# Optimization experiments

Hardware: AMD Instinct MI355X
Metric: run time of the kernel (lower is better)

Reference implementation:

```python
import jax, jax.numpy as jnp
import numpy as np

N_NODES = 50000
N_EDGES = 1600000
H1, F1 = 6, 16   # conv1 heads/filters
H2, F2 = 6, 24   # conv2 heads/filters
D_IN = 11
NEG_SLOPE = 0.2
EPS = 1e-12


def gat_layer(x, src, dst, W, a_src, a_dst, heads, filt):
    # x: [N, Din], W: [Din, heads*filt], a_src/a_dst: [heads, filt]
    N = x.shape[0]
    h = (x @ W).reshape(N, heads, filt)                      # [N,H,F]
    alpha_s = jnp.einsum('nhf,hf->nh', h, a_src)             # [N,H]
    alpha_d = jnp.einsum('nhf,hf->nh', h, a_dst)             # [N,H]
    e = jax.nn.leaky_relu(alpha_s[src] + alpha_d[dst], NEG_SLOPE)  # [E,H]
    # softmax over incoming edges of each dst node (segment softmax)
    m = jax.ops.segment_max(e, dst, num_segments=N)          # [N,H]
    m = jnp.where(jnp.isfinite(m), m, 0.0)
    ex = jnp.exp(e - m[dst])                                 # [E,H]
    denom = jax.ops.segment_sum(ex, dst, num_segments=N)     # [N,H]
    att = ex / (denom[dst] + EPS)                            # [E,H]
    msg = h[src] * att[:, :, None]                           # [E,H,F]
    out = jax.ops.segment_sum(msg, dst, num_segments=N)      # [N,H,F]
    return jax.nn.elu(out).reshape(N, heads * filt)


def setup_inputs() -> dict:
    key = jax.random.key(0)
    ks = jax.random.split(key, 12)
    x = jax.random.normal(ks[0], (N_NODES, D_IN), dtype=jnp.float32)
    src = jax.random.randint(ks[1], (N_EDGES,), 0, N_NODES, dtype=jnp.int32)
    dst = jax.random.randint(ks[2], (N_EDGES,), 0, N_NODES, dtype=jnp.int32)
    s = 0.1
    W1 = jax.random.normal(ks[3], (D_IN, H1 * F1), dtype=jnp.float32) * s
    a1s = jax.random.normal(ks[4], (H1, F1), dtype=jnp.float32) * s
    a1d = jax.random.normal(ks[5], (H1, F1), dtype=jnp.float32) * s
    W2 = jax.random.normal(ks[6], (H1 * F1, H2 * F2), dtype=jnp.float32) * s
    a2s = jax.random.normal(ks[7], (H2, F2), dtype=jnp.float32) * s
    a2d = jax.random.normal(ks[8], (H2, F2), dtype=jnp.float32) * s
    Wd = jax.random.normal(ks[9], (H2 * F2, 1), dtype=jnp.float32) * s
    bd = jnp.zeros((1,), dtype=jnp.float32)
    return {"x": x, "src": src, "dst": dst, "W1": W1, "a1s": a1s, "a1d": a1d,
            "W2": W2, "a2s": a2s, "a2d": a2d, "Wd": Wd, "bd": bd}


def reference(x, src, dst, W1, a1s, a1d, W2, a2s, a2d, Wd, bd):
    h = gat_layer(x, src, dst, W1, a1s, a1d, H1, F1)   # [N, 96]
    h = gat_layer(h, src, dst, W2, a2s, a2d, H2, F2)   # [N, 144]
    pooled = jnp.sum(h, axis=0).reshape(1, -1)         # [1, 144]
    norm = jnp.sqrt(jnp.sum(pooled * pooled, axis=1, keepdims=True))
    pooled = pooled / jnp.maximum(norm, 1e-12)         # F.normalize
    out = pooled @ Wd + bd                             # [1, 1], linear nonlin
    return jnp.squeeze(out, axis=1)                    # [1]
```

## Files before the change

kernel.cpp:

```cpp
#include <hip/hip_runtime.h>
#include <math.h>

#define NNODES 50000
#define NEDGES 1600000
#define NB 391
#define NBP 400

__device__ __forceinline__ float lrelu(float v) { return v > 0.f ? v : 0.2f * v; }

template<int SEL>
__device__ __forceinline__ float fp8d(unsigned u) {
    return __builtin_amdgcn_cvt_f32_fp8((int)u, SEL);
}

__global__ void prep_kernel(const float* __restrict__ x, float* __restrict__ xp,
                            const float* __restrict__ W1, const float* __restrict__ a1s,
                            const float* __restrict__ a1d, float* __restrict__ va1s,
                            float* __restrict__ va1d,
                            const float* __restrict__ W2, const float* __restrict__ a2s,
                            const float* __restrict__ a2d, float* __restrict__ va2s,
                            float* __restrict__ va2d,
                            int* __restrict__ bcnt, float* __restrict__ pooled, int N) {
    int b = blockIdx.x, t = threadIdx.x;
    if (b == 0) {
        if (t < 96) {
            int k = t >> 3, h = t & 7;
            float s = 0.f, d = 0.f;
            if (h < 6 && k < 11) {
                for (int f = 0; f < 16; ++f) {
                    float w = W1[k * 96 + h * 16 + f];
                    s = fmaf(w, a1s[h * 16 + f], s);
                    d = fmaf(w, a1d[h * 16 + f], d);
                }
            }
            va1s[t] = s;
            va1d[t] = d;
        }
    } else if (b == 1) {
        if (t < 768) {
            int k = t >> 3, h = t & 7;
            float s = 0.f, d = 0.f;
            if (h < 6) {
                for (int f = 0; f < 24; ++f) {
                    float w = W2[k * 144 + h * 24 + f];
                    s = fmaf(w, a2s[h * 24 + f], s);
                    d = fmaf(w, a2d[h * 24 + f], d);
                }
            }
            va2s[t] = s;
            va2d[t] = d;
        }
    } else if (b == 2) {
        if (t < NB) bcnt[t] = 0;
        if (t >= 512 && t < 512 + 144) pooled[t - 512] = 0.f;
    } else {
        int i = (b - 3) * 768 + t;
        if (i < N * 12) {
            int n = i / 12, k = i - n * 12;
            xp[i] = (k < 11) ? x[n * 11 + k] : 0.f;
        }
    }
}

template<int DIN>
__global__ void alphap_kernel(const float* __restrict__ X, const float* __restrict__ va_s,
                              const float* __restrict__ va_d, float* __restrict__ asp,
                              float* __restrict__ adp, int N) {
    __shared__ float vs[DIN * 8], vd[DIN * 8];
    for (int i = threadIdx.x; i < DIN * 8; i += blockDim.x) { vs[i] = va_s[i]; vd[i] = va_d[i]; }
    __syncthreads();
    int t = blockIdx.x * blockDim.x + threadIdx.x;
    if (t >= N * 8) return;
    int n = t / 8, h = t - n * 8;
    const float* xr = X + (size_t)n * DIN;
    float s = 0.f, d = 0.f;
    for (int k = 0; k < DIN; ++k) {
        float xv = xr[k];
        s = fmaf(xv, vs[k * 8 + h], s);
        d = fmaf(xv, vd[k * 8 + h], d);
    }
    asp[t] = s;
    adp[t] = d;
}

__global__ void bucket_hist_kernel(const int* __restrict__ dst, int* __restrict__ bcnt, int E) {
    __shared__ int h[NBP];
    for (int i = threadIdx.x; i < NBP; i += blockDim.x) h[i] = 0;
    __syncthreads();
    for (int e = blockIdx.x * blockDim.x + threadIdx.x; e < E; e += gridDim.x * blockDim.x)
        atomicAdd(&h[dst[e] >> 7], 1);
    __syncthreads();
    for (int i = threadIdx.x; i < NB; i += blockDim.x)
        if (h[i]) atomicAdd(&bcnt[i], h[i]);
}

__global__ void bucket_scan_kernel(const int* __restrict__ bcnt, int* __restrict__ bbase,
                                   int* __restrict__ bcur, int* __restrict__ off, int E) {
    __shared__ int ls[512];
    int t = threadIdx.x;
    int c = (t < NB) ? bcnt[t] : 0;
    ls[t] = c;
    __syncthreads();
    for (int o = 1; o < 512; o <<= 1) {
        int u = (t >= o) ? ls[t - o] : 0;
        __syncthreads();
        ls[t] += u;
        __syncthreads();
    }
    if (t < NB) {
        int ex = ls[t] - c;
        bbase[t] = ex;
        bcur[t] = ex;
    }
    if (t == 0) { bbase[NB] = E; off[NNODES] = E; }
}

#define BA_CHUNK 8192
#define BA_THREADS 1024
__global__ void binA_kernel(const int* __restrict__ src, const int* __restrict__ dst,
                            int* __restrict__ bcur, unsigned* __restrict__ tmp, int E) {
    __shared__ unsigned sv[BA_CHUNK];
    __shared__ unsigned short sb[BA_CHUNK];
    __shared__ int cnt[NBP], basel[NBP];
    int tid = threadIdx.x;
    for (int i = tid; i < NBP; i += BA_THREADS) cnt[i] = 0;
    __syncthreads();
    int e0 = blockIdx.x * BA_CHUNK;
    int lim = min(BA_CHUNK, E - e0);
#pragma unroll
    for (int k = 0; k < BA_CHUNK / BA_THREADS; ++k) {
        int i = k * BA_THREADS + tid;
        if (i < lim) {
            int s = src[e0 + i], d = dst[e0 + i];
            sv[i] = (unsigned)s | ((unsigned)(d & 127) << 17);
            int b = d >> 7;
            sb[i] = (unsigned short)b;
            atomicAdd(&cnt[b], 1);
        }
    }
    __syncthreads();
    for (int i = tid; i < NB; i += BA_THREADS)
        basel[i] = cnt[i] ? atomicAdd(&bcur[i], cnt[i]) : 0;
    __syncthreads();
#pragma unroll
    for (int k = 0; k < BA_CHUNK / BA_THREADS; ++k) {
        int i = k * BA_THREADS + tid;
        if (i < lim) {
            int pos = atomicAdd(&basel[sb[i]], 1);
            tmp[pos] = sv[i];
        }
    }
}

__global__ void binB_kernel(const int* __restrict__ bbase, const unsigned* __restrict__ tmp,
                            int* __restrict__ off, int* __restrict__ esrc, int N) {
    __shared__ int ncnt[128], ncur[128], ls[128];
    int b = blockIdx.x;
    int tid = threadIdx.x;
    int lo = bbase[b], hi = bbase[b + 1];
    if (tid < 128) ncnt[tid] = 0;
    __syncthreads();
    for (int i = lo + tid; i < hi; i += 256)
        atomicAdd(&ncnt[tmp[i] >> 17], 1);
    __syncthreads();
    if (tid < 128) ls[tid] = ncnt[tid];
    __syncthreads();
    for (int o = 1; o < 128; o <<= 1) {
        int u = (tid >= o && tid < 128) ? ls[tid - o] : 0;
        __syncthreads();
        if (tid < 128) ls[tid] += u;
        __syncthreads();
    }
    if (tid < 128) {
        int ex = lo + ls[tid] - ncnt[tid];
        int n = b * 128 + tid;
        if (n < N) off[n] = ex;
        ncur[tid] = ex;
    }
    __syncthreads();
    for (int i = lo + tid; i < hi; i += 256) {
        unsigned v = tmp[i];
        int pos = atomicAdd(&ncur[v >> 17], 1);
        esrc[pos] = (int)(v & 0x1FFFFu);
    }
}

#define G1_NODES 128
#define G1_THREADS (G1_NODES * 3)
#define G1_ECAP 4800
__global__ void gather1_kernel(const int* __restrict__ off, const int* __restrict__ esrc,
                               const float* __restrict__ asp, const float* __restrict__ adp,
                               const float* __restrict__ xp, float* __restrict__ aggX, int N) {
    __shared__ int se[G1_ECAP];
    int li = threadIdx.x;
    int n0 = blockIdx.x * G1_NODES;
    int nend = min(n0 + G1_NODES, N);
    int base = off[n0];
    int cnt = off[nend] - base;
    bool staged = (cnt <= G1_ECAP);
    if (staged) for (int i = li; i < cnt; i += G1_THREADS) se[i] = esrc[base + i];
    __syncthreads();
    int node = n0 + li / 3;
    int j = li % 3;
    if (node >= N) return;
    const float4 advA = *(const float4*)(adp + (size_t)node * 8);
    const float2 advB = *(const float2*)(adp + (size_t)node * 8 + 4);
    const float4* xp4 = (const float4*)xp;
    int p0 = off[node], p1 = off[node + 1];
    float4 ac[6];
    float d[6];
#pragma unroll
    for (int u = 0; u < 6; ++u) { ac[u] = make_float4(0.f, 0.f, 0.f, 0.f); d[u] = 0.f; }
#define G1_EDGE(asA, asB, xv)                                                        \
    {                                                                                \
        float a0 = __expf(lrelu(asA.x + advA.x));                                    \
        float a1 = __expf(lrelu(asA.y + advA.y));                                    \
        float a2 = __expf(lrelu(asA.z + advA.z));                                    \
        float a3 = __expf(lrelu(asA.w + advA.w));                                    \
        float a4 = __expf(lrelu(asB.x + advB.x));                                    \
        float a5 = __expf(lrelu(asB.y + advB.y));                                    \
        d[0] += a0; d[1] += a1; d[2] += a2; d[3] += a3; d[4] += a4; d[5] += a5;      \
        ac[0].x = fmaf(a0, xv.x, ac[0].x); ac[0].y = fmaf(a0, xv.y, ac[0].y);        \
        ac[0].z = fmaf(a0, xv.z, ac[0].z); ac[0].w = fmaf(a0, xv.w, ac[0].w);        \
        ac[1].x = fmaf(a1, xv.x, ac[1].x); ac[1].y = fmaf(a1, xv.y, ac[1].y);        \
        ac[1].z = fmaf(a1, xv.z, ac[1].z); ac[1].w = fmaf(a1, xv.w, ac[1].w);        \
        ac[2].x = fmaf(a2, xv.x, ac[2].x); ac[2].y = fmaf(a2, xv.y, ac[2].y);        \
        ac[2].z = fmaf(a2, xv.z, ac[2].z); ac[2].w = fmaf(a2, xv.w, ac[2].w);        \
        ac[3].x = fmaf(a3, xv.x, ac[3].x); ac[3].y = fmaf(a3, xv.y, ac[3].y);        \
        ac[3].z = fmaf(a3, xv.z, ac[3].z); ac[3].w = fmaf(a3, xv.w, ac[3].w);        \
        ac[4].x = fmaf(a4, xv.x, ac[4].x); ac[4].y = fmaf(a4, xv.y, ac[4].y);        \
        ac[4].z = fmaf(a4, xv.z, ac[4].z); ac[4].w = fmaf(a4, xv.w, ac[4].w);        \
        ac[5].x = fmaf(a5, xv.x, ac[5].x); ac[5].y = fmaf(a5, xv.y, ac[5].y);        \
        ac[5].z = fmaf(a5, xv.z, ac[5].z); ac[5].w = fmaf(a5, xv.w, ac[5].w);        \
    }
#define G1_LOOP(FS)                                                                  \
    {                                                                                \
        for (; q + 4 <= qe; q += 4) {                                                \
            int s0 = FS(q), s1 = FS(q + 1), s2 = FS(q + 2), s3 = FS(q + 3);          \
            float4 A0 = *(const float4*)(asp + (size_t)s0 * 8);                      \
            float2 B0 = *(const float2*)(asp + (size_t)s0 * 8 + 4);                  \
            float4 X0 = xp4[(size_t)s0 * 3 + j];                                     \
            float4 A1 = *(const float4*)(asp + (size_t)s1 * 8);                      \
            float2 B1 = *(const float2*)(asp + (size_t)s1 * 8 + 4);                  \
            float4 X1 = xp4[(size_t)s1 * 3 + j];                                     \
            float4 A2 = *(const float4*)(asp + (size_t)s2 * 8);                      \
            float2 B2 = *(const float2*)(asp + (size_t)s2 * 8 + 4);                  \
            float4 X2 = xp4[(size_t)s2 * 3 + j];                                     \
            float4 A3 = *(const float4*)(asp + (size_t)s3 * 8);                      \
            float2 B3 = *(const float2*)(asp + (size_t)s3 * 8 + 4);                  \
            float4 X3 = xp4[(size_t)s3 * 3 + j];                                     \
            G1_EDGE(A0, B0, X0) G1_EDGE(A1, B1, X1)                                  \
            G1_EDGE(A2, B2, X2) G1_EDGE(A3, B3, X3)                                  \
        }                                                                            \
        for (; q < qe; ++q) {                                                        \
            int s0 = FS(q);                                                          \
            float4 A0 = *(const float4*)(asp + (size_t)s0 * 8);                      \
            float2 B0 = *(const float2*)(asp + (size_t)s0 * 8 + 4);                  \
            float4 X0 = xp4[(size_t)s0 * 3 + j];                                     \
            G1_EDGE(A0, B0, X0)                                                      \
        }                                                                            \
    }
#define G1_SE(i) se[i]
#define G1_GE(i) esrc[i]
    if (staged) {
        int q = p0 - base, qe = p1 - base;
        G1_LOOP(G1_SE)
    } else {
        int q = p0, qe = p1;
        G1_LOOP(G1_GE)
    }
#undef G1_EDGE
#undef G1_LOOP
    float4* o4 = (float4*)aggX;
#pragma unroll
    for (int u = 0; u < 6; ++u) {
        float r = 1.f / (d[u] + 1e-12f);
        float4 a = ac[u];
        a.x *= r; a.y *= r; a.z *= r; a.w *= r;
        o4[((size_t)node * 6 + u) * 3 + j] = a;
    }
}

__global__ void gemmL1_kernel(const float* __restrict__ aggX, const float* __restrict__ W1,
                              float* __restrict__ out1, int N) {
    __shared__ float Wl[12 * 96];
    for (int i = threadIdx.x; i < 12 * 96; i += blockDim.x) Wl[i] = (i < 11 * 96) ? W1[i] : 0.f;
    __syncthreads();
    int t = blockIdx.x * blockDim.x + threadIdx.x;
    if (t >= N * 24) return;
    int n = t / 24, q = t - n * 24;
    int h = q / 4, c = q * 4;
    const float* ag = aggX + ((size_t)n * 6 + h) * 12;
    float4 acc = {0, 0, 0, 0};
#pragma unroll
    for (int k = 0; k < 12; ++k) {
        float xv = ag[k];
        acc.x = fmaf(xv, Wl[k * 96 + c + 0], acc.x);
        acc.y = fmaf(xv, Wl[k * 96 + c + 1], acc.y);
        acc.z = fmaf(xv, Wl[k * 96 + c + 2], acc.z);
        acc.w = fmaf(xv, Wl[k * 96 + c + 3], acc.w);
    }
    acc.x = acc.x > 0.f ? acc.x : expm1f(acc.x);
    acc.y = acc.y > 0.f ? acc.y : expm1f(acc.y);
    acc.z = acc.z > 0.f ? acc.z : expm1f(acc.z);
    acc.w = acc.w > 0.f ? acc.w : expm1f(acc.w);
    ((float4*)out1)[(size_t)n * 24 + q] = acc;
}

template<int DIN, int C, int NPT>
__global__ void gemm_fp8_kernel(const float* __restrict__ X, const float* __restrict__ W,
                                unsigned* __restrict__ Out, int N) {
    constexpr int Q = C / 4;
    __shared__ float4 Wl[DIN * Q];
    for (int i = threadIdx.x; i < DIN * Q; i += blockDim.x) Wl[i] = ((const float4*)W)[i];
    __syncthreads();
    int t = blockIdx.x * blockDim.x + threadIdx.x;
    int g = t / Q, q = t - g * Q;
    int n0 = g * NPT;
    if (n0 >= N) return;
    const float4* X4 = (const float4*)X;
    float4 acc[NPT];
#pragma unroll
    for (int u = 0; u < NPT; ++u) acc[u] = make_float4(0.f, 0.f, 0.f, 0.f);
#pragma unroll 2
    for (int k4 = 0; k4 < DIN / 4; ++k4) {
        float4 xv[NPT];
#pragma unroll
        for (int u = 0; u < NPT; ++u) xv[u] = X4[(size_t)(n0 + u) * (DIN / 4) + k4];
#pragma unroll
        for (int i = 0; i < 4; ++i) {
            float4 w = Wl[(k4 * 4 + i) * Q + q];
#pragma unroll
            for (int u = 0; u < NPT; ++u) {
                float xs = (i == 0) ? xv[u].x : (i == 1) ? xv[u].y : (i == 2) ? xv[u].z : xv[u].w;
                acc[u].x = fmaf(xs, w.x, acc[u].x);
                acc[u].y = fmaf(xs, w.y, acc[u].y);
                acc[u].z = fmaf(xs, w.z, acc[u].z);
                acc[u].w = fmaf(xs, w.w, acc[u].w);
            }
        }
    }
#pragma unroll
    for (int u = 0; u < NPT; ++u) {
        int pk = __builtin_amdgcn_cvt_pk_fp8_f32(acc[u].x, acc[u].y, 0, false);
        pk     = __builtin_amdgcn_cvt_pk_fp8_f32(acc[u].z, acc[u].w, pk, true);
        Out[(size_t)(n0 + u) * Q + q] = (unsigned)pk;
    }
}

#define G2_NODES 28
#define G2_TPN 18
#define G2_THREADS 512
#define G2_ACTIVE (G2_NODES * G2_TPN)
#define G2_ECAP 1600
__global__ void gather2_kernel(const int* __restrict__ off, const int* __restrict__ esrc,
                               const float* __restrict__ asp, const float* __restrict__ adp,
                               const uint2* __restrict__ h2t2, float* __restrict__ pooled, int N) {
    __shared__ float sp[144];
    __shared__ int se[G2_ECAP];
    int li = threadIdx.x;
    int n0 = blockIdx.x * G2_NODES;
    int nend = min(n0 + G2_NODES, N);
    int base = off[n0];
    int cnt = off[nend] - base;
    bool staged = (cnt <= G2_ECAP);
    if (staged) for (int i = li; i < cnt; i += G2_THREADS) se[i] = esrc[base + i];
    if (li < 144) sp[li] = 0.f;
    __syncthreads();
    int node = n0 + li / G2_TPN;
    int j = li % G2_TPN;
    if (li < G2_ACTIVE && node < N) {
        int h = j / 3;
        float adv = adp[(size_t)node * 8 + h];
        int p0 = off[node], p1 = off[node + 1];
        float acc[8];
#pragma unroll
        for (int c = 0; c < 8; ++c) acc[c] = 0.f;
        float den = 0.f;
#define G2_EDGE(ev, v)                                                     \
    {                                                                      \
        float att = __expf(lrelu(ev + adv));                               \
        den += att;                                                        \
        acc[0] = fmaf(att, fp8d<0>(v.x), acc[0]);                          \
        acc[1] = fmaf(att, fp8d<1>(v.x), acc[1]);                          \
        acc[2] = fmaf(att, fp8d<2>(v.x), acc[2]);                          \
        acc[3] = fmaf(att, fp8d<3>(v.x), acc[3]);                          \
        acc[4] = fmaf(att, fp8d<0>(v.y), acc[4]);                          \
        acc[5] = fmaf(att, fp8d<1>(v.y), acc[5]);                          \
        acc[6] = fmaf(att, fp8d<2>(v.y), acc[6]);                          \
        acc[7] = fmaf(att, fp8d<3>(v.y), acc[7]);                          \
    }
#define G2_LOOP(FS)                                                                        \
    {                                                                                      \
        for (; q + 4 <= qe; q += 4) {                                                      \
            int s0 = FS(q), s1 = FS(q + 1), s2 = FS(q + 2), s3 = FS(q + 3);                \
            float e0 = asp[(size_t)s0 * 8 + h], e1 = asp[(size_t)s1 * 8 + h];              \
            float e2 = asp[(size_t)s2 * 8 + h], e3 = asp[(size_t)s3 * 8 + h];              \
            uint2 v0 = h2t2[(size_t)s0 * 18 + j], v1 = h2t2[(size_t)s1 * 18 + j];          \
            uint2 v2 = h2t2[(size_t)s2 * 18 + j], v3 = h2t2[(size_t)s3 * 18 + j];          \
            G2_EDGE(e0, v0) G2_EDGE(e1, v1) G2_EDGE(e2, v2) G2_EDGE(e3, v3)                \
        }                                                                                  \
        for (; q < qe; ++q) {                                                              \
            int s0 = FS(q);                                                                \
            float e0 = asp[(size_t)s0 * 8 + h];                                            \
            uint2 v0 = h2t2[(size_t)s0 * 18 + j];                                          \
            G2_EDGE(e0, v0)                                                                \
        }                                                                                  \
    }
#define G2_SE(i) se[i]
#define G2_GE(i) esrc[i]
        if (staged) {
            int q = p0 - base, qe = p1 - base;
            G2_LOOP(G2_SE)
        } else {
            int q = p0, qe = p1;
            G2_LOOP(G2_GE)
        }
#undef G2_EDGE
#undef G2_LOOP
        float rd = 1.f / (den + 1e-12f);
        int cb = 8 * j;
#pragma unroll
        for (int c = 0; c < 8; ++c) {
            float vv = acc[c] * rd;
            vv = vv > 0.f ? vv : expm1f(vv);
            atomicAdd(&sp[cb + c], vv);
        }
    }
    __syncthreads();
    if (li < 144) atomicAdd(&pooled[li], sp[li]);
}

__global__ void final_kernel(const float* __restrict__ pooled, const float* __restrict__ Wd,
                             const float* __restrict__ bd, float* __restrict__ out) {
    int l = threadIdx.x;
    float ss = 0.f, dot = 0.f;
    for (int c = l; c < 144; c += 64) {
        float p = pooled[c];
        ss = fmaf(p, p, ss);
        dot = fmaf(p, Wd[c], dot);
    }
#pragma unroll
    for (int o = 32; o > 0; o >>= 1) {
        ss += __shfl_down(ss, o);
        dot += __shfl_down(dot, o);
    }
    if (l == 0) out[0] = dot / fmaxf(sqrtf(ss), 1e-12f) + bd[0];
}

extern "C" void kernel_launch(void* const* d_in, const int* in_sizes, int n_in,
                              void* d_out, int out_size, void* d_ws, size_t ws_size,
                              hipStream_t stream) {
    const float* x   = (const float*)d_in[0];
    const int*   src = (const int*)  d_in[1];
    const int*   dst = (const int*)  d_in[2];
    const float* W1  = (const float*)d_in[3];
    const float* a1s = (const float*)d_in[4];
    const float* a1d = (const float*)d_in[5];
    const float* W2  = (const float*)d_in[6];
    const float* a2s = (const float*)d_in[7];
    const float* a2d = (const float*)d_in[8];
    const float* Wd  = (const float*)d_in[9];
    const float* bd  = (const float*)d_in[10];

    const int N = NNODES, E = NEDGES;
    float* ws = (float*)d_ws;
    float* xp    = ws;
    float* asp1  = xp + (size_t)N * 12;
    float* adp1  = asp1 + (size_t)N * 8;
    float* aggX  = adp1 + (size_t)N * 8;
    float* out1  = aggX + (size_t)N * 72;
    unsigned* h2t = (unsigned*)(out1 + (size_t)N * 96);
    float* asp2  = out1 + (size_t)N * 96 + (size_t)N * 72;
    float* adp2  = asp2 + (size_t)N * 8;
    float* va1s  = adp2 + (size_t)N * 8;
    float* va1d  = va1s + 96;
    float* va2s  = va1d + 96;
    float* va2d  = va2s + 768;
    float* pooled = va2d + 768;
    int*   off   = (int*)(pooled + 144);
    int*   esrc  = off + (N + 1);
    unsigned* tmp = (unsigned*)(esrc + E);
    int*   bcnt  = (int*)(tmp + E);
    int*   bbase = bcnt + NB;
    int*   bcur  = bbase + (NB + 1);

    const int B = 256;
    auto grid = [](long total, int b) { return (int)((total + b - 1) / b); };

    prep_kernel<<<3 + grid((long)N * 12, 768), 768, 0, stream>>>(
        x, xp, W1, a1s, a1d, va1s, va1d, W2, a2s, a2d, va2s, va2d, bcnt, pooled, N);

    bucket_hist_kernel<<<256, 256, 0, stream>>>(dst, bcnt, E);
    bucket_scan_kernel<<<1, 512, 0, stream>>>(bcnt, bbase, bcur, off, E);
    binA_kernel<<<grid(E, BA_CHUNK), BA_THREADS, 0, stream>>>(src, dst, bcur, tmp, E);
    binB_kernel<<<NB, 256, 0, stream>>>(bbase, tmp, off, esrc, N);

    alphap_kernel<12><<<grid((long)N * 8, B), B, 0, stream>>>(xp, va1s, va1d, asp1, adp1, N);
    gather1_kernel<<<grid(N, G1_NODES), G1_THREADS, 0, stream>>>(off, esrc, asp1, adp1, xp, aggX, N);
    gemmL1_kernel<<<grid((long)N * 24, B), B, 0, stream>>>(aggX, W1, out1, N);

    alphap_kernel<96><<<grid((long)N * 8, B), B, 0, stream>>>(out1, va2s, va2d, asp2, adp2, N);
    gemm_fp8_kernel<96, 144, 2><<<grid((long)(N / 2) * 36, 1024), 1024, 0, stream>>>(out1, W2, h2t, N);
    gather2_kernel<<<grid(N, G2_NODES), G2_THREADS, 0, stream>>>(off, esrc, asp2, adp2,
                                                                 (const uint2*)h2t, pooled, N);

    final_kernel<<<1, 64, 0, stream>>>(pooled, Wd, bd, (float*)d_out);
}
```

Before: 215.5 us.

## Fuse layer-1 GEMM, layer-2 alpha projection and fp8 GEMM into one kernel

Replaces three kernels (the layer-1 projection with ELU, the layer-2 attention-logit projection, and the layer-2 fp8 GEMM) with one kernel. Each 1024-thread block handles 28 nodes and keeps the layer-1 output in shared memory, so out1 is never written to or re-read from global memory. It also saves two launches. In exchange each block reloads about 62KB of weights into LDS, which limits occupancy, and roughly 16 threads per block sit idle.

```diff
diff --git a/kernel.cpp b/kernel.cpp
--- a/kernel.cpp
+++ b/kernel.cpp
@@ -281,70 +281,62 @@
     }
 }
 
-__global__ void gemmL1_kernel(const float* __restrict__ aggX, const float* __restrict__ W1,
-                              float* __restrict__ out1, int N) {
-    __shared__ float Wl[12 * 96];
-    for (int i = threadIdx.x; i < 12 * 96; i += blockDim.x) Wl[i] = (i < 11 * 96) ? W1[i] : 0.f;
-    __syncthreads();
-    int t = blockIdx.x * blockDim.x + threadIdx.x;
-    if (t >= N * 24) return;
-    int n = t / 24, q = t - n * 24;
-    int h = q / 4, c = q * 4;
-    const float* ag = aggX + ((size_t)n * 6 + h) * 12;
-    float4 acc = {0, 0, 0, 0};
-#pragma unroll
-    for (int k = 0; k < 12; ++k) {
-        float xv = ag[k];
-        acc.x = fmaf(xv, Wl[k * 96 + c + 0], acc.x);
-        acc.y = fmaf(xv, Wl[k * 96 + c + 1], acc.y);
-        acc.z = fmaf(xv, Wl[k * 96 + c + 2], acc.z);
-        acc.w = fmaf(xv, Wl[k * 96 + c + 3], acc.w);
-    }
-    acc.x = acc.x > 0.f ? acc.x : expm1f(acc.x);
-    acc.y = acc.y > 0.f ? acc.y : expm1f(acc.y);
-    acc.z = acc.z > 0.f ? acc.z : expm1f(acc.z);
-    acc.w = acc.w > 0.f ? acc.w : expm1f(acc.w);
-    ((float4*)out1)[(size_t)n * 24 + q] = acc;
-}
-
-template<int DIN, int C, int NPT>
-__global__ void gemm_fp8_kernel(const float* __restrict__ X, const float* __restrict__ W,
-                                unsigned* __restrict__ Out, int N) {
-    constexpr int Q = C / 4;
-    __shared__ float4 Wl[DIN * Q];
-    for (int i = threadIdx.x; i < DIN * Q; i += blockDim.x) Wl[i] = ((const float4*)W)[i];
-    __syncthreads();
-    int t = blockIdx.x * blockDim.x + threadIdx.x;
-    int g = t / Q, q = t - g * Q;
-    int n0 = g * NPT;
-    if (n0 >= N) return;
-    const float4* X4 = (const float4*)X;
-    float4 acc[NPT];
-#pragma unroll
-    for (int u = 0; u < NPT; ++u) acc[u] = make_float4(0.f, 0.f, 0.f, 0.f);
-#pragma unroll 2
-    for (int k4 = 0; k4 < DIN / 4; ++k4) {
-        float4 xv[NPT];
-#pragma unroll
-        for (int u = 0; u < NPT; ++u) xv[u] = X4[(size_t)(n0 + u) * (DIN / 4) + k4];
-#pragma unroll
-        for (int i = 0; i < 4; ++i) {
-            float4 w = Wl[(k4 * 4 + i) * Q + q];
-#pragma unroll
-            for (int u = 0; u < NPT; ++u) {
-                float xs = (i == 0) ? xv[u].x : (i == 1) ? xv[u].y : (i == 2) ? xv[u].z : xv[u].w;
-                acc[u].x = fmaf(xs, w.x, acc[u].x);
-                acc[u].y = fmaf(xs, w.y, acc[u].y);
-                acc[u].z = fmaf(xs, w.z, acc[u].z);
-                acc[u].w = fmaf(xs, w.w, acc[u].w);
-            }
-        }
-    }
-#pragma unroll
-    for (int u = 0; u < NPT; ++u) {
-        int pk = __builtin_amdgcn_cvt_pk_fp8_f32(acc[u].x, acc[u].y, 0, false);
-        pk     = __builtin_amdgcn_cvt_pk_fp8_f32(acc[u].z, acc[u].w, pk, true);
-        Out[(size_t)(n0 + u) * Q + q] = (unsigned)pk;
+#define FL_G 28
+#define FL_THREADS 1024
+__global__ __launch_bounds__(FL_THREADS) void fusedL2_kernel(
+        const float* __restrict__ aggX, const float* __restrict__ W1,
+        const float* __restrict__ W2, const float* __restrict__ va2s_g,
+        const float* __restrict__ va2d_g, float* __restrict__ asp2,
+        float* __restrict__ adp2, unsigned* __restrict__ h2t, int N) {
+    __shared__ float W1l[12 * 96];
+    __shared__ float4 W2l[96 * 36];
+    __shared__ float v2s[768], v2d[768];
+    __shared__ float o1[FL_G][100];
+    int t = threadIdx.x;
+    for (int i = t; i < 12 * 96; i += FL_THREADS) W1l[i] = (i < 11 * 96) ? W1[i] : 0.f;
+    for (int i = t; i < 96 * 36; i += FL_THREADS) W2l[i] = ((const float4*)W2)[i];
+    for (int i = t; i < 768; i += FL_THREADS) { v2s[i] = va2s_g[i]; v2d[i] = va2d_g[i]; }
+    __syncthreads();
+    int ln = t / 36;
+    int jj = t - ln * 36;
+    int n = blockIdx.x * FL_G + ln;
+    bool act = (ln < FL_G) && (n < N);
+    if (act && jj < 32) {
+#pragma unroll
+        for (int cc = 0; cc < 3; ++cc) {
+            int c = jj * 3 + cc;
+            int h = c >> 4;
+            const float* ag = aggX + (size_t)n * 72 + h * 12;
+            float acc = 0.f;
+#pragma unroll
+            for (int k = 0; k < 12; ++k) acc = fmaf(ag[k], W1l[k * 96 + c], acc);
+            o1[ln][c] = acc > 0.f ? acc : expm1f(acc);
+        }
+    }
+    __syncthreads();
+    if (act && jj < 12) {
+        int h = jj >> 1;
+        bool isd = jj & 1;
+        const float* vv = isd ? v2d : v2s;
+        float acc = 0.f;
+#pragma unroll 8
+        for (int k = 0; k < 96; ++k) acc = fmaf(o1[ln][k], vv[k * 8 + h], acc);
+        (isd ? adp2 : asp2)[(size_t)n * 8 + h] = acc;
+    }
+    if (act) {
+        float4 acc = {0.f, 0.f, 0.f, 0.f};
+#pragma unroll 8
+        for (int k = 0; k < 96; ++k) {
+            float xv = o1[ln][k];
+            float4 w = W2l[k * 36 + jj];
+            acc.x = fmaf(xv, w.x, acc.x);
+            acc.y = fmaf(xv, w.y, acc.y);
+            acc.z = fmaf(xv, w.z, acc.z);
+            acc.w = fmaf(xv, w.w, acc.w);
+        }
+        int pk = __builtin_amdgcn_cvt_pk_fp8_f32(acc.x, acc.y, 0, false);
+        pk     = __builtin_amdgcn_cvt_pk_fp8_f32(acc.z, acc.w, pk, true);
+        h2t[(size_t)n * 36 + jj] = (unsigned)pk;
     }
 }
 
@@ -498,10 +490,10 @@
 
     alphap_kernel<12><<<grid((long)N * 8, B), B, 0, stream>>>(xp, va1s, va1d, asp1, adp1, N);
     gather1_kernel<<<grid(N, G1_NODES), G1_THREADS, 0, stream>>>(off, esrc, asp1, adp1, xp, aggX, N);
-    gemmL1_kernel<<<grid((long)N * 24, B), B, 0, stream>>>(aggX, W1, out1, N);
-
-    alphap_kernel<96><<<grid((long)N * 8, B), B, 0, stream>>>(out1, va2s, va2d, asp2, adp2, N);
-    gemm_fp8_kernel<96, 144, 2><<<grid((long)(N / 2) * 36, 1024), 1024, 0, stream>>>(out1, W2, h2t, N);
+
+    fusedL2_kernel<<<grid(N, FL_G), FL_THREADS, 0, stream>>>(
+        aggX, W1, W2, va2s, va2d, asp2, adp2, h2t, N);
+
     gather2_kernel<<<grid(N, G2_NODES), G2_THREADS, 0, stream>>>(off, esrc, asp2, adp2,
                                                                  (const uint2*)h2t, pooled, N);
 
```

Result: slower. 240.4 us (+11.5%).

## Split layer-2 gather into three head-pair passes over planar fp8 features

Applied to the files above, without the earlier changes.

Reorganizes the layer-2 fp8 feature table and source attention scores into three planar slices of two heads each, and runs the gather kernel three times, once per slice. Each pass reads a feature working set about a third the size (48 bytes per node), so the random source-node gathers are more likely to hit in L2/MALL. In exchange the CSR edge list and offsets are read three times, there are two extra launches, and each block now covers 84 nodes with 6 threads per node.

```diff
diff --git a/kernel.cpp b/kernel.cpp
--- a/kernel.cpp
+++ b/kernel.cpp
@@ -81,6 +81,26 @@
     }
     asp[t] = s;
     adp[t] = d;
+}
+
+__global__ void alphap2_kernel(const float* __restrict__ X, const float* __restrict__ va_s,
+                               const float* __restrict__ va_d, float* __restrict__ aspP,
+                               float* __restrict__ adp, int N) {
+    __shared__ float vs[768], vd[768];
+    for (int i = threadIdx.x; i < 768; i += blockDim.x) { vs[i] = va_s[i]; vd[i] = va_d[i]; }
+    __syncthreads();
+    int t = blockIdx.x * blockDim.x + threadIdx.x;
+    if (t >= N * 8) return;
+    int n = t / 8, h = t - n * 8;
+    const float* xr = X + (size_t)n * 96;
+    float s = 0.f, d = 0.f;
+    for (int k = 0; k < 96; ++k) {
+        float xv = xr[k];
+        s = fmaf(xv, vs[k * 8 + h], s);
+        d = fmaf(xv, vd[k * 8 + h], d);
+    }
+    adp[t] = d;
+    if (h < 6) aspP[(size_t)(h >> 1) * N * 2 + (size_t)n * 2 + (h & 1)] = s;
 }
 
 __global__ void bucket_hist_kernel(const int* __restrict__ dst, int* __restrict__ bcnt, int E) {
@@ -340,23 +360,25 @@
             }
         }
     }
+    int pass = q / 12, idx = q - pass * 12;
 #pragma unroll
     for (int u = 0; u < NPT; ++u) {
         int pk = __builtin_amdgcn_cvt_pk_fp8_f32(acc[u].x, acc[u].y, 0, false);
         pk     = __builtin_amdgcn_cvt_pk_fp8_f32(acc[u].z, acc[u].w, pk, true);
-        Out[(size_t)(n0 + u) * Q + q] = (unsigned)pk;
-    }
-}
-
-#define G2_NODES 28
-#define G2_TPN 18
+        Out[(size_t)pass * N * 12 + (size_t)(n0 + u) * 12 + idx] = (unsigned)pk;
+    }
+}
+
+#define G2_NODES 84
+#define G2_TPN 6
 #define G2_THREADS 512
 #define G2_ACTIVE (G2_NODES * G2_TPN)
-#define G2_ECAP 1600
+#define G2_ECAP 4096
 __global__ void gather2_kernel(const int* __restrict__ off, const int* __restrict__ esrc,
-                               const float* __restrict__ asp, const float* __restrict__ adp,
-                               const uint2* __restrict__ h2t2, float* __restrict__ pooled, int N) {
-    __shared__ float sp[144];
+                               const float* __restrict__ aspP, const float* __restrict__ adp,
+                               const uint2* __restrict__ h2p2, float* __restrict__ pooled,
+                               int N, int pass) {
+    __shared__ float sp[48];
     __shared__ int se[G2_ECAP];
     int li = threadIdx.x;
     int n0 = blockIdx.x * G2_NODES;
@@ -365,13 +387,13 @@
     int cnt = off[nend] - base;
     bool staged = (cnt <= G2_ECAP);
     if (staged) for (int i = li; i < cnt; i += G2_THREADS) se[i] = esrc[base + i];
-    if (li < 144) sp[li] = 0.f;
+    if (li < 48) sp[li] = 0.f;
     __syncthreads();
     int node = n0 + li / G2_TPN;
     int j = li % G2_TPN;
     if (li < G2_ACTIVE && node < N) {
-        int h = j / 3;
-        float adv = adp[(size_t)node * 8 + h];
+        int hl = j / 3;
+        float adv = adp[(size_t)node * 8 + 2 * pass + hl];
         int p0 = off[node], p1 = off[node + 1];
         float acc[8];
 #pragma unroll
@@ -394,16 +416,16 @@
     {                                                                                      \
         for (; q + 4 <= qe; q += 4) {                                                      \
             int s0 = FS(q), s1 = FS(q + 1), s2 = FS(q + 2), s3 = FS(q + 3);                \
-            float e0 = asp[(size_t)s0 * 8 + h], e1 = asp[(size_t)s1 * 8 + h];              \
-            float e2 = asp[(size_t)s2 * 8 + h], e3 = asp[(size_t)s3 * 8 + h];              \
-            uint2 v0 = h2t2[(size_t)s0 * 18 + j], v1 = h2t2[(size_t)s1 * 18 + j];          \
-            uint2 v2 = h2t2[(size_t)s2 * 18 + j], v3 = h2t2[(size_t)s3 * 18 + j];          \
+            float e0 = aspP[(size_t)s0 * 2 + hl], e1 = aspP[(size_t)s1 * 2 + hl];          \
+            float e2 = aspP[(size_t)s2 * 2 + hl], e3 = aspP[(size_t)s3 * 2 + hl];          \
+            uint2 v0 = h2p2[(size_t)s0 * 6 + j], v1 = h2p2[(size_t)s1 * 6 + j];            \
+            uint2 v2 = h2p2[(size_t)s2 * 6 + j], v3 = h2p2[(size_t)s3 * 6 + j];            \
             G2_EDGE(e0, v0) G2_EDGE(e1, v1) G2_EDGE(e2, v2) G2_EDGE(e3, v3)                \
         }                                                                                  \
         for (; q < qe; ++q) {                                                              \
             int s0 = FS(q);                                                                \
-            float e0 = asp[(size_t)s0 * 8 + h];                                            \
-            uint2 v0 = h2t2[(size_t)s0 * 18 + j];                                          \
+            float e0 = aspP[(size_t)s0 * 2 + hl];                                          \
+            uint2 v0 = h2p2[(size_t)s0 * 6 + j];                                           \
             G2_EDGE(e0, v0)                                                                \
         }                                                                                  \
     }
@@ -428,7 +450,7 @@
         }
     }
     __syncthreads();
-    if (li < 144) atomicAdd(&pooled[li], sp[li]);
+    if (li < 48) atomicAdd(&pooled[pass * 48 + li], sp[li]);
 }
 
 __global__ void final_kernel(const float* __restrict__ pooled, const float* __restrict__ Wd,
@@ -471,8 +493,8 @@
     float* aggX  = adp1 + (size_t)N * 8;
     float* out1  = aggX + (size_t)N * 72;
     unsigned* h2t = (unsigned*)(out1 + (size_t)N * 96);
-    float* asp2  = out1 + (size_t)N * 96 + (size_t)N * 72;
-    float* adp2  = asp2 + (size_t)N * 8;
+    float* aspP  = out1 + (size_t)N * 96 + (size_t)N * 72;
+    float* adp2  = aspP + (size_t)N * 8;
     float* va1s  = adp2 + (size_t)N * 8;
     float* va1d  = va1s + 96;
     float* va2s  = va1d + 96;
@@ -500,10 +522,14 @@
     gather1_kernel<<<grid(N, G1_NODES), G1_THREADS, 0, stream>>>(off, esrc, asp1, adp1, xp, aggX, N);
     gemmL1_kernel<<<grid((long)N * 24, B), B, 0, stream>>>(aggX, W1, out1, N);
 
-    alphap_kernel<96><<<grid((long)N * 8, B), B, 0, stream>>>(out1, va2s, va2d, asp2, adp2, N);
+    alphap2_kernel<<<grid((long)N * 8, B), B, 0, stream>>>(out1, va2s, va2d, aspP, adp2, N);
     gemm_fp8_kernel<96, 144, 2><<<grid((long)(N / 2) * 36, 1024), 1024, 0, stream>>>(out1, W2, h2t, N);
-    gather2_kernel<<<grid(N, G2_NODES), G2_THREADS, 0, stream>>>(off, esrc, asp2, adp2,
-                                                                 (const uint2*)h2t, pooled, N);
+
+    for (int pass = 0; pass < 3; ++pass) {
+        gather2_kernel<<<grid(N, G2_NODES), G2_THREADS, 0, stream>>>(
+            off, esrc, aspP + (size_t)pass * N * 2, adp2,
+            (const uint2*)(h2t + (size_t)pass * N * 12), pooled, N, pass);
+    }
 
     final_kernel<<<1, 64, 0, stream>>>(pooled, Wd, bd, (float*)d_out);
 }
```

Measured after the change: 253.9 us. 1.18x slower.
